# Kernel tuning notes

Hardware: AMD Instinct MI355X
Metric: run time of the kernel (lower is better)

Reference implementation:

```python
import jax, jax.numpy as jnp
import numpy as np

V, E, H, N, L = 32000, 512, 512, 64, 128


def setup_inputs() -> dict:
    key = jax.random.key(0)
    ks = jax.random.split(key, 16)
    s = 0.02  # init scale
    return {
        "input_ids": jax.random.randint(ks[0], (N,), 0, V),
        "h": jax.random.normal(ks[1], (N, H), jnp.float32),
        "c": jax.random.normal(ks[2], (N, H), jnp.float32),
        "encoder_hiddens": jax.random.normal(ks[3], (N, L, H), jnp.float32),
        "attn_mask": jnp.zeros((N, L), dtype=bool),
        "embed_W": jax.random.normal(ks[4], (V, E), jnp.float32) * s,
        "w_ih": jax.random.normal(ks[5], (4 * H, E), jnp.float32) * s,
        "b_ih": jnp.zeros((4 * H,), jnp.float32),
        "w_hh": jax.random.normal(ks[6], (4 * H, H), jnp.float32) * s,
        "b_hh": jnp.zeros((4 * H,), jnp.float32),
        "attn_Wh": jax.random.normal(ks[7], (H, H), jnp.float32) * s,
        "attn_Ws": jax.random.normal(ks[8], (H, H), jnp.float32) * s,
        "attn_v": jax.random.normal(ks[9], (H,), jnp.float32) * s,
        "h2o_W": jax.random.normal(ks[10], (V, 2 * H), jnp.float32) * s,
        "h2o_b": jnp.zeros((V,), jnp.float32),
    }


def reference(input_ids, h, c, encoder_hiddens, attn_mask, embed_W,
              w_ih, b_ih, w_hh, b_hh, attn_Wh, attn_Ws, attn_v,
              h2o_W, h2o_b):
    # Embedding lookup: (N, E)
    emb = embed_W[input_ids]
    # LSTM cell: fused gate GEMMs, chunk order i, f, g, o (torch chunk(4))
    gates = emb @ w_ih.T + b_ih + h @ w_hh.T + b_hh  # (N, 4H)
    i_g, f_g, g_g, o_g = jnp.split(gates, 4, axis=1)
    c_t = jax.nn.sigmoid(f_g) * c + jax.nn.sigmoid(i_g) * jnp.tanh(g_g)
    h_t = jax.nn.sigmoid(o_g) * jnp.tanh(c_t)  # (N, H)
    # Bahdanau attention: v^T tanh(W_h h_t + W_s enc)
    proj = jnp.tanh((h_t @ attn_Wh.T)[:, None, :] + encoder_hiddens @ attn_Ws.T)  # (N, L, H)
    score = jnp.einsum('nlh,h->nl', proj, attn_v)  # (N, L)
    score = jnp.where(attn_mask, -jnp.inf, score)
    attn_w = jax.nn.softmax(score, axis=1)  # (N, L)
    context = jnp.einsum('nl,nlh->nh', attn_w, encoder_hiddens)  # (N, H)
    # Output projection + log-softmax over vocab
    combined = jnp.concatenate([h_t, context], axis=1)  # (N, 2H)
    out = jax.nn.log_softmax(combined @ h2o_W.T + h2o_b, axis=-1)  # (N, V)
    return out, h_t, c_t
```

## Files before the change

### kernel.cpp

```cpp
#include <hip/hip_runtime.h>
#include <hip/hip_bf16.h>
#include <math.h>

#define V 32000
#define E 512
#define H 512
#define N 64
#define L 128
#define NV (N*V)
#define NH (N*H)
#define MTOT (N*L)
#define VT 500

typedef short  s8v  __attribute__((ext_vector_type(8)));
typedef float  f4v  __attribute__((ext_vector_type(4)));

__device__ __forceinline__ float sigf(float x) { return 1.0f / (1.0f + __expf(-x)); }

__device__ __forceinline__ unsigned short f2bf(float f) {
    unsigned int u = __float_as_uint(f);
    unsigned int r = u + 0x7FFFu + ((u >> 16) & 1u);
    return (unsigned short)(r >> 16);
}

__device__ __forceinline__ unsigned int cvt2bf(float x, float y) {
    __hip_bfloat162 h2 = __float22bfloat162_rn(make_float2(x, y));
    unsigned int r;
    __builtin_memcpy(&r, &h2, 4);
    return r;
}

__device__ __forceinline__ uint4 pack_q(float4 lo, float4 hi) {
    uint4 q;
    q.x = cvt2bf(lo.x, lo.y); q.y = cvt2bf(lo.z, lo.w);
    q.z = cvt2bf(hi.x, hi.y); q.w = cvt2bf(hi.z, hi.w);
    return q;
}

__global__ __launch_bounds__(256) void k_gates(
    const int* __restrict__ ids, const float* __restrict__ hprev,
    const float* __restrict__ embW, const float* __restrict__ w_ih,
    const float* __restrict__ w_hh, float* __restrict__ gates_p)
{
    __shared__ __align__(16) float xs[64 * 128];
    const int bx = blockIdx.x;
    const int ks = blockIdx.y;
    const int tid = threadIdx.x;
    const bool emb_part = (ks < 4);
    const int koff = (ks & 3) * 128;

    for (int i = tid; i < 64 * 32; i += 256) {
        int n = i >> 5, kk4 = i & 31;
        float4 x4;
        if (emb_part)
            x4 = ((const float4*)(embW + (size_t)ids[n] * E + koff))[kk4];
        else
            x4 = ((const float4*)(hprev + (size_t)n * H + koff))[kk4];
        ((float4*)xs)[n * 32 + kk4] = x4;
    }
    __syncthreads();

    const int jl = tid & 63;
    const int ng = tid >> 6;
    const int j = bx * 64 + jl;
    const int nb = ng * 16;
    const float* wrow = (emb_part ? w_ih : w_hh) + (size_t)j * 512 + koff;

    float acc[16];
#pragma unroll
    for (int i = 0; i < 16; ++i) acc[i] = 0.f;

    for (int e4 = 0; e4 < 32; ++e4) {
        float4 w4 = ((const float4*)wrow)[e4];
#pragma unroll
        for (int i = 0; i < 16; ++i) {
            float4 x4 = ((const float4*)xs)[(nb + i) * 32 + e4];
            acc[i] += w4.x * x4.x + w4.y * x4.y + w4.z * x4.z + w4.w * x4.w;
        }
    }
#pragma unroll
    for (int i = 0; i < 16; ++i)
        gates_p[(size_t)ks * (64 * 2048) + (size_t)(nb + i) * 2048 + j] = acc[i];
}

__global__ __launch_bounds__(256) void k_lstm_pw(
    const float* __restrict__ gates_p, const float* __restrict__ b_ih,
    const float* __restrict__ b_hh, const float* __restrict__ cprev,
    float* __restrict__ out, unsigned short* __restrict__ xb)
{
    int i = blockIdx.x * 256 + threadIdx.x;
    if (i >= NH) return;
    int n = i >> 9, k = i & 511;
    float g[4];
#pragma unroll
    for (int q = 0; q < 4; ++q) {
        int j = q * 512 + k;
        float s = b_ih[j] + b_hh[j];
#pragma unroll
        for (int ks = 0; ks < 8; ++ks)
            s += gates_p[(size_t)ks * (64 * 2048) + (size_t)n * 2048 + j];
        g[q] = s;
    }
    float ig = sigf(g[0]), fg = sigf(g[1]), gg = tanhf(g[2]), og = sigf(g[3]);
    float ct = fg * cprev[i] + ig * gg;
    float ht = og * tanhf(ct);
    out[NV + i] = ht;
    out[NV + NH + i] = ct;
    xb[(size_t)n * 1024 + k] = f2bf(ht);
}

__global__ __launch_bounds__(256) void k_sproj(
    const float* __restrict__ out, const float* __restrict__ Wh,
    float* __restrict__ sproj)
{
    __shared__ __align__(16) float xs[512];
    int n = blockIdx.x >> 1;
    int h = (blockIdx.x & 1) * 256 + threadIdx.x;
    const float* ht = out + NV + (size_t)n * 512;
    for (int i = threadIdx.x; i < 512; i += 256) xs[i] = ht[i];
    __syncthreads();
    const float* wrow = Wh + (size_t)h * 512;
    float acc = 0.f;
    for (int e4 = 0; e4 < 128; ++e4) {
        float4 w4 = ((const float4*)wrow)[e4];
        float4 x4 = ((const float4*)xs)[e4];
        acc += w4.x * x4.x + w4.y * x4.y + w4.z * x4.z + w4.w * x4.w;
    }
    sproj[(size_t)n * 512 + h] = acc;
}

__global__ __launch_bounds__(256) void k_score_gemm(
    const float* __restrict__ enc, const float* __restrict__ Ws,
    const float* __restrict__ sproj, const float* __restrict__ av,
    float* __restrict__ scorep)
{
    __shared__ __align__(16) short As[64 * 72];
    __shared__ __align__(16) short Bs[64 * 72];
    __shared__ float sred[64];

    const int bh = blockIdx.x, bm = blockIdx.y;
    const int tid = threadIdx.x;
    const int w = tid >> 6, l = tid & 63;
    const int wave_m = (w >> 1) * 32, wave_h = (w & 1) * 32;
    const int lq = l >> 4, lr = l & 15;

    if (tid < 64) sred[tid] = 0.f;

    f4v acc[2][2];
#pragma unroll
    for (int i = 0; i < 2; ++i)
#pragma unroll
        for (int j = 0; j < 2; ++j) acc[i][j] = (f4v)0.f;

    for (int kt = 0; kt < 8; ++kt) {
        __syncthreads();
#pragma unroll
        for (int r = 0; r < 2; ++r) {
            int idx = (r * 256 + tid) * 8;
            int row = idx >> 6, col = idx & 63;
            const float* sa = enc + (size_t)(bm * 64 + row) * 512 + kt * 64 + col;
            const float* sb = Ws  + (size_t)(bh * 64 + row) * 512 + kt * 64 + col;
            float4 a0 = *(const float4*)sa, a1 = *(const float4*)(sa + 4);
            float4 b0 = *(const float4*)sb, b1 = *(const float4*)(sb + 4);
            *(uint4*)(As + row * 72 + col) = pack_q(a0, a1);
            *(uint4*)(Bs + row * 72 + col) = pack_q(b0, b1);
        }
        __syncthreads();

#pragma unroll
        for (int ks = 0; ks < 2; ++ks) {
            s8v a_frag[2], b_frag[2];
#pragma unroll
            for (int i = 0; i < 2; ++i)
                a_frag[i] = *(const s8v*)(As + (wave_m + 16 * i + lr) * 72 + ks * 32 + lq * 8);
#pragma unroll
            for (int j = 0; j < 2; ++j)
                b_frag[j] = *(const s8v*)(Bs + (wave_h + 16 * j + lr) * 72 + ks * 32 + lq * 8);
#pragma unroll
            for (int i = 0; i < 2; ++i)
#pragma unroll
                for (int j = 0; j < 2; ++j)
                    acc[i][j] = __builtin_amdgcn_mfma_f32_16x16x32_bf16(
                        a_frag[i], b_frag[j], acc[i][j], 0, 0, 0);
        }
    }
    __syncthreads();

    const int hc0 = bh * 64 + wave_h + lr;
#pragma unroll
    for (int i = 0; i < 2; ++i) {
#pragma unroll
        for (int reg = 0; reg < 4; ++reg) {
            int m_local = wave_m + 16 * i + lq * 4 + reg;
            int m = bm * 64 + m_local;
            int n = m >> 7;
            float p = 0.f;
#pragma unroll
            for (int j = 0; j < 2; ++j) {
                int hc = hc0 + 16 * j;
                float val = acc[i][j][reg] + sproj[(size_t)n * 512 + hc];
                p += tanhf(val) * av[hc];
            }
            p += __shfl_xor(p, 1, 64);
            p += __shfl_xor(p, 2, 64);
            p += __shfl_xor(p, 4, 64);
            p += __shfl_xor(p, 8, 64);
            if (lr == 0) atomicAdd(&sred[m_local], p);
        }
    }
    __syncthreads();
    if (tid < 64)
        scorep[(size_t)bh * MTOT + bm * 64 + tid] = sred[tid];
}

__global__ __launch_bounds__(128) void k_softmax_ctx(
    const float* __restrict__ scorep, const unsigned char* __restrict__ mask,
    const float* __restrict__ enc, unsigned short* __restrict__ xb)
{
    __shared__ float wl[128];
    __shared__ float red[4];
    const int n = blockIdx.x, hc = blockIdx.y, t = threadIdx.x;

    float s = 0.f;
#pragma unroll
    for (int q = 0; q < 8; ++q)
        s += scorep[(size_t)q * MTOT + n * 128 + t];
    if (mask[(size_t)n * 128 + t]) s = -1e30f;

    float m = s;
#pragma unroll
    for (int off = 32; off > 0; off >>= 1) m = fmaxf(m, __shfl_xor(m, off, 64));
    if ((t & 63) == 0) red[t >> 6] = m;
    __syncthreads();
    m = fmaxf(red[0], red[1]);
    float e = __expf(s - m);
    float ss = e;
#pragma unroll
    for (int off = 32; off > 0; off >>= 1) ss += __shfl_xor(ss, off, 64);
    if ((t & 63) == 0) red[2 + (t >> 6)] = ss;
    __syncthreads();
    float inv = 1.0f / (red[2] + red[3]);
    wl[t] = e * inv;
    __syncthreads();

    const float* encn = enc + (size_t)n * (L * H) + hc * 128 + t;
    float acc = 0.f;
#pragma unroll 8
    for (int ll = 0; ll < 128; ++ll)
        acc += wl[ll] * encn[(size_t)ll * 512];
    xb[(size_t)n * 1024 + 512 + hc * 128 + t] = f2bf(acc);
}

__global__ __launch_bounds__(512) void k_logits(
    const float* __restrict__ h2oW, const unsigned short* __restrict__ xb,
    const float* __restrict__ h2ob, float* __restrict__ dlogits,
    float* __restrict__ pmax, float* __restrict__ psum)
{
    __shared__ __align__(16) short As[2][64 * 72];
    __shared__ __align__(16) short Bs[2][64 * 72];
    __shared__ __align__(16) float cs[64 * 68];

    const int bm = blockIdx.x;
    const int tid = threadIdx.x;
    const int g = tid >> 8;
    const int tl = tid & 255;
    const int w2 = (tid >> 6) & 3;
    const int l = tid & 63;
    const int wave_m = (w2 & 1) * 32, wave_n = (w2 >> 1) * 32;
    const int lq = l >> 4, lr = l & 15;

    const int arow = tl >> 2;
    const int acol = (tl & 3) * 16;
    const float* aptr = h2oW + (size_t)(bm * 64 + arow) * 1024 + g * 512 + acol;
    const unsigned short* bptr = xb + (size_t)arow * 1024 + g * 512 + acol;

    short* Asg = As[g];
    short* Bsg = Bs[g];

    f4v acc[2][2];
#pragma unroll
    for (int i = 0; i < 2; ++i)
#pragma unroll
        for (int j = 0; j < 2; ++j) acc[i][j] = (f4v)0.f;

#pragma unroll 1
    for (int kt = 0; kt < 8; ++kt) {
        if (kt) __syncthreads();
        const float* ap = aptr + kt * 64;
        const unsigned short* bp = bptr + kt * 64;
        float4 a0 = ((const float4*)ap)[0], a1 = ((const float4*)ap)[1];
        float4 a2 = ((const float4*)ap)[2], a3 = ((const float4*)ap)[3];
        uint4 b0 = *(const uint4*)bp, b1 = *(const uint4*)(bp + 8);
        *(uint4*)(Asg + arow * 72 + acol)     = pack_q(a0, a1);
        *(uint4*)(Asg + arow * 72 + acol + 8) = pack_q(a2, a3);
        *(uint4*)(Bsg + arow * 72 + acol)     = b0;
        *(uint4*)(Bsg + arow * 72 + acol + 8) = b1;
        __syncthreads();

#pragma unroll
        for (int ks = 0; ks < 2; ++ks) {
            s8v a_frag[2], b_frag[2];
#pragma unroll
            for (int i = 0; i < 2; ++i)
                a_frag[i] = *(const s8v*)(Asg + (wave_m + 16 * i + lr) * 72 + ks * 32 + lq * 8);
#pragma unroll
            for (int j = 0; j < 2; ++j)
                b_frag[j] = *(const s8v*)(Bsg + (wave_n + 16 * j + lr) * 72 + ks * 32 + lq * 8);
#pragma unroll
            for (int i = 0; i < 2; ++i)
#pragma unroll
                for (int j = 0; j < 2; ++j)
                    acc[i][j] = __builtin_amdgcn_mfma_f32_16x16x32_bf16(
                        a_frag[i], b_frag[j], acc[i][j], 0, 0, 0);
        }
    }
    __syncthreads();

    if (g == 0) {
#pragma unroll
        for (int i = 0; i < 2; ++i)
#pragma unroll
            for (int j = 0; j < 2; ++j)
#pragma unroll
                for (int reg = 0; reg < 4; ++reg)
                    cs[(wave_n + 16 * j + lr) * 68 + wave_m + 16 * i + lq * 4 + reg] = acc[i][j][reg];
    }
    __syncthreads();
    if (g == 1) {
#pragma unroll
        for (int i = 0; i < 2; ++i)
#pragma unroll
            for (int j = 0; j < 2; ++j)
#pragma unroll
                for (int reg = 0; reg < 4; ++reg)
                    cs[(wave_n + 16 * j + lr) * 68 + wave_m + 16 * i + lq * 4 + reg] += acc[i][j][reg];
    }
    __syncthreads();

    if (tid < 256) {
        const int n = tid >> 2, q = tid & 3;
        const int v0 = bm * 64 + q * 16;
        float4 vals[4];
        float m_loc = -1e30f;
#pragma unroll
        for (int k = 0; k < 4; ++k) {
            float4 cv = *(const float4*)(cs + n * 68 + q * 16 + 4 * k);
            float4 bv = *(const float4*)(h2ob + v0 + 4 * k);
            cv.x += bv.x; cv.y += bv.y; cv.z += bv.z; cv.w += bv.w;
            vals[k] = cv;
            *(float4*)(dlogits + (size_t)n * V + v0 + 4 * k) = cv;
            m_loc = fmaxf(m_loc, fmaxf(fmaxf(cv.x, cv.y), fmaxf(cv.z, cv.w)));
        }
        float s_loc = 0.f;
#pragma unroll
        for (int k = 0; k < 4; ++k) {
            s_loc += __expf(vals[k].x - m_loc) + __expf(vals[k].y - m_loc)
                   + __expf(vals[k].z - m_loc) + __expf(vals[k].w - m_loc);
        }
        float m2 = fmaxf(m_loc, __shfl_xor(m_loc, 1, 64));
        m2 = fmaxf(m2, __shfl_xor(m2, 2, 64));
        s_loc *= __expf(m_loc - m2);
        float s2 = s_loc + __shfl_xor(s_loc, 1, 64);
        s2 += __shfl_xor(s2, 2, 64);
        if (q == 0) {
            pmax[(size_t)n * VT + bm] = m2;
            psum[(size_t)n * VT + bm] = s2;
        }
    }
}

__global__ __launch_bounds__(256) void k_lse(
    const float* __restrict__ pmax, const float* __restrict__ psum,
    float* __restrict__ lse)
{
    __shared__ float rm[4], rs[4];
    const int n = blockIdx.x, t = threadIdx.x;
    float m0 = (t < VT) ? pmax[(size_t)n * VT + t] : -1e30f;
    float m1 = (t + 256 < VT) ? pmax[(size_t)n * VT + t + 256] : -1e30f;
    float mm = fmaxf(m0, m1);
#pragma unroll
    for (int off = 32; off > 0; off >>= 1) mm = fmaxf(mm, __shfl_xor(mm, off, 64));
    if ((t & 63) == 0) rm[t >> 6] = mm;
    __syncthreads();
    float m = fmaxf(fmaxf(rm[0], rm[1]), fmaxf(rm[2], rm[3]));

    float s = 0.f;
    if (t < VT)       s += psum[(size_t)n * VT + t] * __expf(m0 - m);
    if (t + 256 < VT) s += psum[(size_t)n * VT + t + 256] * __expf(m1 - m);
#pragma unroll
    for (int off = 32; off > 0; off >>= 1) s += __shfl_xor(s, off, 64);
    if ((t & 63) == 0) rs[t >> 6] = s;
    __syncthreads();
    if (t == 0) {
        float st = rs[0] + rs[1] + rs[2] + rs[3];
        lse[n] = m + __logf(st);
    }
}

__global__ __launch_bounds__(256) void k_norm(
    float* __restrict__ dlogits, const float* __restrict__ lse)
{
    const int n = blockIdx.y;
    const int t4 = blockIdx.x * 256 + threadIdx.x;
    if (t4 >= V / 4) return;
    float s = lse[n];
    float4* p = (float4*)(dlogits + (size_t)n * V) + t4;
    float4 v = *p;
    v.x -= s; v.y -= s; v.z -= s; v.w -= s;
    *p = v;
}

extern "C" void kernel_launch(void* const* d_in, const int* in_sizes, int n_in,
                              void* d_out, int out_size, void* d_ws, size_t ws_size,
                              hipStream_t stream)
{
    const int* ids   = (const int*)d_in[0];
    const float* h   = (const float*)d_in[1];
    const float* c   = (const float*)d_in[2];
    const float* enc = (const float*)d_in[3];
    const unsigned char* mask = (const unsigned char*)d_in[4];
    const float* embW = (const float*)d_in[5];
    const float* w_ih = (const float*)d_in[6];
    const float* b_ih = (const float*)d_in[7];
    const float* w_hh = (const float*)d_in[8];
    const float* b_hh = (const float*)d_in[9];
    const float* Wh   = (const float*)d_in[10];
    const float* Ws   = (const float*)d_in[11];
    const float* av   = (const float*)d_in[12];
    const float* h2oW = (const float*)d_in[13];
    const float* h2ob = (const float*)d_in[14];

    float* out = (float*)d_out;
    float* ws = (float*)d_ws;
    float* gates_p = ws;
    float* sproj   = ws + 1048576;
    float* scorep  = ws + 1048576 + 32768;
    unsigned short* xb = (unsigned short*)(ws + 1048576 + 32768 + 65536);
    float* pmax = ws;
    float* psum = ws + 32000;
    float* lse  = ws + 64000;

    k_gates<<<dim3(32, 8), 256, 0, stream>>>(ids, h, embW, w_ih, w_hh, gates_p);
    k_lstm_pw<<<128, 256, 0, stream>>>(gates_p, b_ih, b_hh, c, out, xb);
    k_sproj<<<128, 256, 0, stream>>>(out, Wh, sproj);
    k_score_gemm<<<dim3(8, 128), 256, 0, stream>>>(enc, Ws, sproj, av, scorep);
    k_softmax_ctx<<<dim3(64, 4), 128, 0, stream>>>(scorep, mask, enc, xb);
    k_logits<<<VT, 512, 0, stream>>>(h2oW, xb, h2ob, out, pmax, psum);
    k_lse<<<64, 256, 0, stream>>>(pmax, psum, lse);
    k_norm<<<dim3(32, 64), 256, 0, stream>>>(out, lse);
}
```

Before: 342.4 us.

## Register-tile gates GEMM 4x4 with padded LDS; fuse LSE and normalization kernels

The gates GEMM now gives each thread a 4x4 tile (4 gate columns by 4 batch rows) instead of 1x16. LDS rows are padded to 132 floats to avoid bank conflicts, and results are written as float4 stores. Separately, the log-sum-exp reduction and the subtract-normalization are merged into one kernel launched over (64,8) blocks. Each block recomputes the row LSE redundantly and then normalizes 1000 float4s, which removes one launch and the lse round trip. The cost is duplicated reduction work per chunk and strided weight-row reads in the gates kernel.

Measured after the change: 345.2 us. No clear change (+0.8%).

```diff
diff --git a/kernel.cpp b/kernel.cpp
--- a/kernel.cpp
+++ b/kernel.cpp
@@ -42,7 +42,7 @@
     const float* __restrict__ embW, const float* __restrict__ w_ih,
     const float* __restrict__ w_hh, float* __restrict__ gates_p)
 {
-    __shared__ __align__(16) float xs[64 * 128];
+    __shared__ __align__(16) float xs[64 * 132];
     const int bx = blockIdx.x;
     const int ks = blockIdx.y;
     const int tid = threadIdx.x;
@@ -56,31 +56,45 @@
             x4 = ((const float4*)(embW + (size_t)ids[n] * E + koff))[kk4];
         else
             x4 = ((const float4*)(hprev + (size_t)n * H + koff))[kk4];
-        ((float4*)xs)[n * 32 + kk4] = x4;
-    }
-    __syncthreads();
-
-    const int jl = tid & 63;
-    const int ng = tid >> 6;
-    const int j = bx * 64 + jl;
-    const int nb = ng * 16;
-    const float* wrow = (emb_part ? w_ih : w_hh) + (size_t)j * 512 + koff;
-
-    float acc[16];
-#pragma unroll
-    for (int i = 0; i < 16; ++i) acc[i] = 0.f;
+        ((float4*)xs)[n * 33 + kk4] = x4;
+    }
+    __syncthreads();
+
+    const int jq = tid & 15;
+    const int nq = tid >> 4;
+    const int j0 = jq * 4;
+    const int n0 = nq * 4;
+    const float* wbase = (emb_part ? w_ih : w_hh)
+                       + (size_t)(bx * 64 + j0) * 512 + koff;
+
+    float acc[4][4];
+#pragma unroll
+    for (int nn = 0; nn < 4; ++nn)
+#pragma unroll
+        for (int jj = 0; jj < 4; ++jj) acc[nn][jj] = 0.f;
 
     for (int e4 = 0; e4 < 32; ++e4) {
-        float4 w4 = ((const float4*)wrow)[e4];
-#pragma unroll
-        for (int i = 0; i < 16; ++i) {
-            float4 x4 = ((const float4*)xs)[(nb + i) * 32 + e4];
-            acc[i] += w4.x * x4.x + w4.y * x4.y + w4.z * x4.z + w4.w * x4.w;
-        }
-    }
-#pragma unroll
-    for (int i = 0; i < 16; ++i)
-        gates_p[(size_t)ks * (64 * 2048) + (size_t)(nb + i) * 2048 + j] = acc[i];
+        float4 w4[4];
+#pragma unroll
+        for (int jj = 0; jj < 4; ++jj)
+            w4[jj] = ((const float4*)(wbase + (size_t)jj * 512))[e4];
+        float4 x4[4];
+#pragma unroll
+        for (int nn = 0; nn < 4; ++nn)
+            x4[nn] = ((const float4*)xs)[(n0 + nn) * 33 + e4];
+#pragma unroll
+        for (int nn = 0; nn < 4; ++nn)
+#pragma unroll
+            for (int jj = 0; jj < 4; ++jj)
+                acc[nn][jj] += w4[jj].x * x4[nn].x + w4[jj].y * x4[nn].y
+                             + w4[jj].z * x4[nn].z + w4[jj].w * x4[nn].w;
+    }
+#pragma unroll
+    for (int nn = 0; nn < 4; ++nn) {
+        float4 o = make_float4(acc[nn][0], acc[nn][1], acc[nn][2], acc[nn][3]);
+        *(float4*)(gates_p + (size_t)ks * (64 * 2048)
+                 + (size_t)(n0 + nn) * 2048 + bx * 64 + j0) = o;
+    }
 }
 
 __global__ __launch_bounds__(256) void k_lstm_pw(
@@ -369,12 +383,13 @@
     }
 }
 
-__global__ __launch_bounds__(256) void k_lse(
+__global__ __launch_bounds__(256) void k_lse_norm(
     const float* __restrict__ pmax, const float* __restrict__ psum,
-    float* __restrict__ lse)
+    float* __restrict__ dlogits)
 {
     __shared__ float rm[4], rs[4];
-    const int n = blockIdx.x, t = threadIdx.x;
+    __shared__ float lsev;
+    const int n = blockIdx.x, ch = blockIdx.y, t = threadIdx.x;
     float m0 = (t < VT) ? pmax[(size_t)n * VT + t] : -1e30f;
     float m1 = (t + 256 < VT) ? pmax[(size_t)n * VT + t + 256] : -1e30f;
     float mm = fmaxf(m0, m1);
@@ -393,21 +408,18 @@
     __syncthreads();
     if (t == 0) {
         float st = rs[0] + rs[1] + rs[2] + rs[3];
-        lse[n] = m + __logf(st);
-    }
-}
-
-__global__ __launch_bounds__(256) void k_norm(
-    float* __restrict__ dlogits, const float* __restrict__ lse)
-{
-    const int n = blockIdx.y;
-    const int t4 = blockIdx.x * 256 + threadIdx.x;
-    if (t4 >= V / 4) return;
-    float s = lse[n];
-    float4* p = (float4*)(dlogits + (size_t)n * V) + t4;
-    float4 v = *p;
-    v.x -= s; v.y -= s; v.z -= s; v.w -= s;
-    *p = v;
+        lsev = m + __logf(st);
+    }
+    __syncthreads();
+    const float lse = lsev;
+
+    float4* row = (float4*)(dlogits + (size_t)n * V) + ch * 1000;
+#pragma unroll 2
+    for (int idx = t; idx < 1000; idx += 256) {
+        float4 v = row[idx];
+        v.x -= lse; v.y -= lse; v.z -= lse; v.w -= lse;
+        row[idx] = v;
+    }
 }
 
 extern "C" void kernel_launch(void* const* d_in, const int* in_sizes, int n_in,
@@ -438,7 +450,6 @@
     unsigned short* xb = (unsigned short*)(ws + 1048576 + 32768 + 65536);
     float* pmax = ws;
     float* psum = ws + 32000;
-    float* lse  = ws + 64000;
 
     k_gates<<<dim3(32, 8), 256, 0, stream>>>(ids, h, embW, w_ih, w_hh, gates_p);
     k_lstm_pw<<<128, 256, 0, stream>>>(gates_p, b_ih, b_hh, c, out, xb);
@@ -446,6 +457,5 @@
     k_score_gemm<<<dim3(8, 128), 256, 0, stream>>>(enc, Ws, sproj, av, scorep);
     k_softmax_ctx<<<dim3(64, 4), 128, 0, stream>>>(scorep, mask, enc, xb);
     k_logits<<<VT, 512, 0, stream>>>(h2oW, xb, h2ob, out, pmax, psum);
-    k_lse<<<64, 256, 0, stream>>>(pmax, psum, lse);
-    k_norm<<<dim3(32, 64), 256, 0, stream>>>(out, lse);
-}
+    k_lse_norm<<<dim3(64, 8), 256, 0, stream>>>(pmax, psum, out);
+}
```
